# Performance work log

Hardware: AMD Instinct MI355X
Metric: run time of the kernel (lower is better)

Reference implementation:

```python
import jax, jax.numpy as jnp
import numpy as np

B, M = 32768, 200
NUM_LAYERS, OW, OH = 22, 11, 11
CNN_CH, HIDDEN = 128, 512
ACTION_NVEC = (9, 10)


def setup_inputs() -> dict:
    key = jax.random.key(0)
    ks = jax.random.split(key, 16)
    s = 0.02
    inp = {
        "observations": jax.random.randint(ks[0], (B, M, 3), 0, 256, dtype=jnp.int32),
        "max_vec": jnp.ones((NUM_LAYERS,), dtype=jnp.float32),
        "w_conv1": jax.random.normal(ks[1], (CNN_CH, NUM_LAYERS, 5, 5), jnp.float32) * s,
        "b_conv1": jnp.zeros((CNN_CH,), jnp.float32),
        "w_conv2": jax.random.normal(ks[2], (CNN_CH, CNN_CH, 3, 3), jnp.float32) * s,
        "b_conv2": jnp.zeros((CNN_CH,), jnp.float32),
        "w_fc": jax.random.normal(ks[3], (CNN_CH, HIDDEN // 2), jnp.float32) * s,
        "b_fc": jnp.zeros((HIDDEN // 2,), jnp.float32),
        "w_self": jax.random.normal(ks[4], (NUM_LAYERS, HIDDEN // 2), jnp.float32) * s,
        "b_self": jnp.zeros((HIDDEN // 2,), jnp.float32),
        "w_actor0": jax.random.normal(ks[5], (HIDDEN, ACTION_NVEC[0]), jnp.float32) * 0.01,
        "b_actor0": jnp.zeros((ACTION_NVEC[0],), jnp.float32),
        "w_actor1": jax.random.normal(ks[6], (HIDDEN, ACTION_NVEC[1]), jnp.float32) * 0.01,
        "b_actor1": jnp.zeros((ACTION_NVEC[1],), jnp.float32),
        "w_value": jax.random.normal(ks[7], (HIDDEN, 1), jnp.float32) * s,
        "b_value": jnp.zeros((1,), jnp.float32),
    }
    return inp


def _conv(x, w, b, stride):
    y = jax.lax.conv_general_dilated(
        x, w, window_strides=(stride, stride), padding="VALID",
        dimension_numbers=("NCHW", "OIHW", "NCHW"))
    return y + b[None, :, None, None]


def _encode(observations, max_vec, w_conv1, b_conv1, w_conv2, b_conv2,
            w_fc, b_fc, w_self, b_self):
    # torch: token_observations[token_observations == 255] = 0
    obs = jnp.where(observations == 255, 0, observations)
    coords = obs[..., 0]                       # [B, M]
    x_idx = (coords >> 4) & 15
    y_idx = coords & 15
    atr_idx = obs[..., 1]
    atr_val = obs[..., 2].astype(jnp.float32)
    # coords_byte != 255 is always True after the 255->0 rewrite above
    valid = (x_idx < OW) & (y_idx < OH) & (atr_idx < NUM_LAYERS)
    b_idx = jnp.broadcast_to(jnp.arange(obs.shape[0])[:, None], coords.shape)
    # route invalid tokens to a dummy batch slot B, then drop it
    b_idx = jnp.where(valid, b_idx, obs.shape[0])
    a_idx = jnp.where(valid, atr_idx, 0)
    xs = jnp.where(valid, x_idx, 0)
    ys = jnp.where(valid, y_idx, 0)
    box = jnp.zeros((obs.shape[0] + 1, NUM_LAYERS, OW, OH), jnp.float32)
    box = box.at[b_idx, a_idx, xs, ys].set(atr_val)[: obs.shape[0]]
    features = box / max_vec[None, :, None, None]
    self_feat = jax.nn.relu(features[:, :, 5, 5] @ w_self + b_self)   # [B, 256]
    h = jax.nn.relu(_conv(features, w_conv1, b_conv1, 3))             # [B,128,3,3]
    h = jax.nn.relu(_conv(h, w_conv2, b_conv2, 1))                    # [B,128,1,1]
    h = h.reshape(h.shape[0], -1)                                     # [B,128]
    cnn_feat = jax.nn.relu(h @ w_fc + b_fc)                           # [B,256]
    return jnp.concatenate([self_feat, cnn_feat], axis=1)             # [B,512]


def reference(observations, max_vec, w_conv1, b_conv1, w_conv2, b_conv2,
              w_fc, b_fc, w_self, b_self, w_actor0, b_actor0,
              w_actor1, b_actor1, w_value, b_value):
    hidden = _encode(observations, max_vec, w_conv1, b_conv1, w_conv2, b_conv2,
                     w_fc, b_fc, w_self, b_self)
    logits0 = hidden @ w_actor0 + b_actor0
    logits1 = hidden @ w_actor1 + b_actor1
    value = hidden @ w_value + b_value
    return (logits0, logits1, value, hidden)
```

## Files before the change

kernel.cpp:

```cpp
#include <hip/hip_runtime.h>
#include <hip/hip_bf16.h>

typedef unsigned int uint;
typedef unsigned short ushort;
typedef unsigned long long ull;
typedef __attribute__((ext_vector_type(8))) short short8;
typedef __attribute__((ext_vector_type(4))) float float4_;

#define B_TOT 32768
#define NL    22
#define HID0  ((long)B_TOT * 20)

#define W2F_OFF  0
#define WFCF_OFF 294912
#define WHF_OFF  360448
#define W1P_OFF  393216
#define H1_OFF   534016

__device__ __forceinline__ ushort f2bf(float v) {
  uint x = __float_as_uint(v);
  x += 0x7fffu + ((x >> 16) & 1u);
  return (ushort)(x >> 16);
}
__device__ __forceinline__ uint cvtpk(float lo, float hi) {
  uint r;
  asm volatile("v_cvt_pk_bf16_f32 %0, %1, %2" : "=v"(r) : "v"(lo), "v"(hi));
  return r;
}
struct u3 { uint x, y, z; };

extern "C" __global__ __launch_bounds__(256)
void k_prep(const float* __restrict__ wc1, const float* __restrict__ wc2,
            const float* __restrict__ wfc,
            const float* __restrict__ wa0, const float* __restrict__ wa1,
            const float* __restrict__ wv,
            ushort* __restrict__ w2f, ushort* __restrict__ wfcf,
            ushort* __restrict__ whf, uint* __restrict__ w1p)
{
  int i = blockIdx.x * 256 + threadIdx.x;
  if (i < 18432) {
    int l = i & 63, cg = (i >> 6) & 7, ks = i >> 9;
    int col = cg * 16 + (l & 15), kb = ks * 32 + (l >> 4) * 8;
    ushort t[8];
    #pragma unroll
    for (int j = 0; j < 8; ++j) t[j] = f2bf(wc2[col * 1152 + kb + j]);
    uint4 o = { (uint)t[0]|((uint)t[1]<<16), (uint)t[2]|((uint)t[3]<<16),
                (uint)t[4]|((uint)t[5]<<16), (uint)t[6]|((uint)t[7]<<16) };
    ((uint4*)w2f)[i] = o;
  } else if (i < 22528) {
    int i2 = i - 18432;
    int l = i2 & 63, cg = (i2 >> 6) & 15, ks = i2 >> 10;
    int col = cg * 16 + (l & 15), kb = ks * 32 + (l >> 4) * 8;
    ushort t[8];
    #pragma unroll
    for (int j = 0; j < 8; ++j) t[j] = f2bf(wfc[(kb + j) * 256 + col]);
    uint4 o = { (uint)t[0]|((uint)t[1]<<16), (uint)t[2]|((uint)t[3]<<16),
                (uint)t[4]|((uint)t[5]<<16), (uint)t[6]|((uint)t[7]<<16) };
    ((uint4*)wfcf)[i2] = o;
  } else if (i < 24576) {
    int i2 = i - 22528;
    int l = i2 & 63, cg = (i2 >> 6) & 1, ks = i2 >> 7;
    int col = cg * 16 + (l & 15), kb = ks * 32 + (l >> 4) * 8;
    ushort t[8];
    #pragma unroll
    for (int j = 0; j < 8; ++j) {
      int k = kb + j;
      float v = (col < 9)  ? wa0[k*9 + col]
              : (col < 19) ? wa1[k*10 + (col - 9)]
              : (col == 19) ? wv[k] : 0.f;
      t[j] = f2bf(v);
    }
    uint4 o = { (uint)t[0]|((uint)t[1]<<16), (uint)t[2]|((uint)t[3]<<16),
                (uint)t[4]|((uint)t[5]<<16), (uint)t[6]|((uint)t[7]<<16) };
    ((uint4*)whf)[i2] = o;
  } else if (i < 24576 + 35200) {
    int j = i - 24576;
    int l = j & 63, r = j >> 6;
    ushort lo_ = f2bf(wc1[(2*l)     * 550 + r]);
    ushort hi_ = f2bf(wc1[(2*l + 1) * 550 + r]);
    w1p[j] = (uint)lo_ | ((uint)hi_ << 16);
  }
}

#define PROC(cur, acc0, acc1, sav, sbv)                                    \
  {                                                                        \
    int a = (int)((cur) >> 16), x = (int)(((cur) >> 12) & 15u),            \
        y = (int)(((cur) >> 8) & 15u);                                     \
    float rmv = __int_as_float(                                            \
        __builtin_amdgcn_readlane(__float_as_int(rm_own), a));             \
    float fv = (float)((cur) & 255u) * rmv;                                \
    if (x == 5 && y == 5) {                                                \
      const float2* ws2 = (const float2*)(wself + a * 256);                \
      float2 w0 = ws2[lane], w1 = ws2[64 + lane];                          \
      sav.x = fmaf(fv, w0.x, sav.x);  sav.y = fmaf(fv, w0.y, sav.y);       \
      sbv.x = fmaf(fv, w1.x, sbv.x);  sbv.y = fmaf(fv, w1.y, sbv.y);       \
    }                                                                      \
    const int wbase = a * 25;                                              \
    _Pragma("unroll")                                                      \
    for (int ox = 0; ox < 3; ++ox) {                                       \
      int kx = x - 3 * ox;                                                 \
      if ((unsigned)kx > 4u) continue;                                     \
      _Pragma("unroll")                                                    \
      for (int oy = 0; oy < 3; ++oy) {                                     \
        int ky = y - 3 * oy;                                               \
        if ((unsigned)ky > 4u) continue;                                   \
        uint wu = w1p[(wbase + kx * 5 + ky) * 64 + lane];                  \
        float wx = __uint_as_float(wu << 16);                              \
        float wy = __uint_as_float(wu & 0xffff0000u);                      \
        acc0[ox*3+oy] = fmaf(fv, wx, acc0[ox*3+oy]);                       \
        acc1[ox*3+oy] = fmaf(fv, wy, acc1[ox*3+oy]);                       \
      }                                                                    \
    }                                                                      \
  }

#define EPILOG(bS, acc0, acc1, sav, sbv)                                   \
  {                                                                        \
    const float2* bs2 = (const float2*)bself;                              \
    float2 b0_ = bs2[lane], b1_ = bs2[64 + lane];                          \
    float2 o0 = { fmaxf(sav.x + b0_.x, 0.f), fmaxf(sav.y + b0_.y, 0.f) };  \
    float2 o1 = { fmaxf(sbv.x + b1_.x, 0.f), fmaxf(sbv.y + b1_.y, 0.f) };  \
    float2* out2 = (float2*)(out + HID0 + (bS) * 512);                     \
    out2[lane] = o0;                                                       \
    out2[64 + lane] = o1;                                                  \
    const float2 bc = ((const float2*)bc1)[lane];                          \
    float v0[9], v1[9];                                                    \
    _Pragma("unroll")                                                      \
    for (int p = 0; p < 9; ++p) {                                          \
      v0[p] = fmaxf(acc0[p] + bc.x, 0.f);                                  \
      v1[p] = fmaxf(acc1[p] + bc.y, 0.f);                                  \
    }                                                                      \
    uint wds[9];                                                           \
    wds[0] = cvtpk(v0[0], v0[1]);                                          \
    wds[1] = cvtpk(v0[2], v0[3]);                                          \
    wds[2] = cvtpk(v0[4], v0[5]);                                          \
    wds[3] = cvtpk(v0[6], v0[7]);                                          \
    wds[4] = cvtpk(v0[8], v1[0]);                                          \
    wds[5] = cvtpk(v1[1], v1[2]);                                          \
    wds[6] = cvtpk(v1[3], v1[4]);                                          \
    wds[7] = cvtpk(v1[5], v1[6]);                                          \
    wds[8] = cvtpk(v1[7], v1[8]);                                          \
    uint* dst = (uint*)h1g + (bS) * 576 + 9 * lane;                        \
    _Pragma("unroll")                                                      \
    for (int j = 0; j < 9; ++j) dst[j] = wds[j];                           \
  }

extern "C" __global__ __launch_bounds__(256)
void k_encode(const int* __restrict__ obs, const float* __restrict__ maxvec,
              const uint* __restrict__ w1p, const float* __restrict__ bc1,
              const float* __restrict__ wself, const float* __restrict__ bself,
              float* __restrict__ out, ushort* __restrict__ h1g)
{
  __shared__ uint klist[8][64];

  const int tid = threadIdx.x, lane = tid & 63, w = tid >> 6;
  const long bA = (long)blockIdx.x * 8 + w * 2;
  const long bB = bA + 1;

  float rm_own = (lane < NL) ? (1.0f / maxvec[lane]) : 0.f;

  const uint* obA = (const uint*)obs + bA * 600;
  const uint* obB = (const uint*)obs + bB * 600;
  uint* klA = klist[w * 2 + 0];
  uint* klB = klist[w * 2 + 1];

  int cntA = 0, cntB = 0;
  #pragma unroll
  for (int r = 0; r < 4; ++r) {
    int m = r * 64 + lane;
    bool vA = false, vB = false; uint pkA = 0, pkB = 0;
    if (m < 200) {
      u3 tA = *(const u3*)(obA + m * 3);
      u3 tB = *(const u3*)(obB + m * 3);
      uint cA = tA.x, aA = tA.y, vvA = tA.z;
      uint cB = tB.x, aB = tB.y, vvB = tB.z;
      cA = (cA == 255u) ? 0u : cA;  aA = (aA == 255u) ? 0u : aA;  vvA = (vvA == 255u) ? 0u : vvA;
      cB = (cB == 255u) ? 0u : cB;  aB = (aB == 255u) ? 0u : aB;  vvB = (vvB == 255u) ? 0u : vvB;
      uint xA = (cA >> 4) & 15u, yA = cA & 15u;
      uint xB = (cB >> 4) & 15u, yB = cB & 15u;
      vA = (xA < 11u) && (yA < 11u) && (aA < NL);
      vB = (xB < 11u) && (yB < 11u) && (aB < NL);
      pkA = (aA << 16) | (xA << 12) | (yA << 8) | vvA;
      pkB = (aB << 16) | (xB << 12) | (yB << 8) | vvB;
    }
    ull balA = __ballot(vA);
    if (vA) {
      int pos = cntA + __popcll(balA & ((1ull << lane) - 1ull));
      if (pos < 64) klA[pos] = pkA;
    }
    cntA += __popcll(balA);
    ull balB = __ballot(vB);
    if (vB) {
      int pos = cntB + __popcll(balB & ((1ull << lane) - 1ull));
      if (pos < 64) klB[pos] = pkB;
    }
    cntB += __popcll(balB);
  }
  if (cntA > 64) cntA = 64;
  if (cntB > 64) cntB = 64;

  uint uA = (lane < cntA) ? klA[lane] : 0xffffffffu;
  uint uB = (lane < cntB) ? klB[lane] : 0xffffffffu;
  uint cellA = uA >> 8, cellB = uB >> 8;
  bool aliveA = (lane < cntA), aliveB = (lane < cntB);
  const int dmax = (cntA > cntB) ? cntA : cntB;
  for (int d = 1; d < dmax; ++d) {
    uint oA = __shfl_down(cellA, d);
    uint oB = __shfl_down(cellB, d);
    aliveA = aliveA && !((lane + d < cntA) && (oA == cellA));
    aliveB = aliveB && !((lane + d < cntB) && (oB == cellB));
  }
  ull balA2 = __ballot(aliveA);
  const int n2A = __popcll(balA2);
  if (aliveA) klA[__popcll(balA2 & ((1ull << lane) - 1ull))] = uA;
  ull balB2 = __ballot(aliveB);
  const int n2B = __popcll(balB2);
  if (aliveB) klB[__popcll(balB2 & ((1ull << lane) - 1ull))] = uB;

  float aA0[9] = {0,0,0,0,0,0,0,0,0}, aA1[9] = {0,0,0,0,0,0,0,0,0};
  float aB0[9] = {0,0,0,0,0,0,0,0,0}, aB1[9] = {0,0,0,0,0,0,0,0,0};
  float2 saA = {0.f,0.f}, sbA = {0.f,0.f}, saB = {0.f,0.f}, sbB = {0.f,0.f};
  const int tmax = (n2A > n2B) ? n2A : n2B;
  uint nxtA = klA[0], nxtB = klB[0];
  for (int t = 0; t < tmax; ++t) {
    uint curvA = nxtA, curvB = nxtB;
    nxtA = klA[(t + 1) & 63];
    nxtB = klB[(t + 1) & 63];
    uint curA = (uint)__builtin_amdgcn_readfirstlane((int)curvA);
    uint curB = (uint)__builtin_amdgcn_readfirstlane((int)curvB);
    if (t < n2A) PROC(curA, aA0, aA1, saA, sbA);
    if (t < n2B) PROC(curB, aB0, aB1, saB, sbB);
  }

  EPILOG(bA, aA0, aA1, saA, sbA);
  EPILOG(bB, aB0, aB1, saB, sbB);
}

extern "C" __global__ __launch_bounds__(256)
void k_mlp(const ushort* __restrict__ h1g, const ushort* __restrict__ w2f,
           const float* __restrict__ bc2, const ushort* __restrict__ wfcf,
           const float* __restrict__ bfc, const ushort* __restrict__ whf,
           const float* __restrict__ ba0, const float* __restrict__ ba1,
           const float* __restrict__ bv, float* __restrict__ out)
{
  __shared__ short  Abuf[2][4][64][8];
  __shared__ ushort h2A[16][64][8];

  const int tid = threadIdx.x, lane = tid & 63, w = tid >> 6;
  const int lo = lane & 15, hi = lane >> 4;
  const int bb = blockIdx.x, b0 = bb * 64;

  const short8* w2fv  = (const short8*)w2f;
  const short8* wfcfv = (const short8*)wfcf;
  const uint4*  A4    = (const uint4*)h1g;
  const long    arow  = (long)(b0 + (tid >> 2)) * 144 + (tid & 3);

  float4_ acc[4][2];
  #pragma unroll
  for (int cgi = 0; cgi < 2; ++cgi) {
    float bv_ = bc2[(2*w + cgi)*16 + lo];
    float4_ t = {bv_, bv_, bv_, bv_};
    #pragma unroll
    for (int m = 0; m < 4; ++m) acc[m][cgi] = t;
  }

  uint4 rA = A4[arow];
  for (int t = 0; t < 36; ++t) {
    const int cur = t & 1;
    *(uint4*)&Abuf[cur][tid & 3][tid >> 2][0] = rA;
    if (t + 1 < 36) rA = A4[arow + (t + 1) * 4];
    __syncthreads();
    short8 af[4];
    #pragma unroll
    for (int m = 0; m < 4; ++m)
      af[m] = *(const short8*)&Abuf[cur][hi][m*16 + lo][0];
    #pragma unroll
    for (int cgi = 0; cgi < 2; ++cgi) {
      short8 bf = w2fv[(t*8 + 2*w + cgi)*64 + lane];
      #pragma unroll
      for (int m = 0; m < 4; ++m)
        acc[m][cgi] = __builtin_amdgcn_mfma_f32_16x16x32_bf16(af[m], bf, acc[m][cgi], 0, 0, 0);
    }
  }
  __syncthreads();

  #pragma unroll
  for (int cgi = 0; cgi < 2; ++cgi) {
    int col = (2*w + cgi)*16 + lo;
    #pragma unroll
    for (int m = 0; m < 4; ++m)
      #pragma unroll
      for (int q = 0; q < 4; ++q) {
        int R = m*16 + hi*4 + q;
        h2A[col >> 3][R][col & 7] = f2bf(fmaxf(acc[m][cgi][q], 0.f));
      }
  }
  __syncthreads();

  float4_ acc2[4][4];
  #pragma unroll
  for (int cgi = 0; cgi < 4; ++cgi) {
    float bv_ = bfc[(4*w + cgi)*16 + lo];
    float4_ t = {bv_, bv_, bv_, bv_};
    #pragma unroll
    for (int m = 0; m < 4; ++m) acc2[m][cgi] = t;
  }
  #pragma unroll
  for (int ks = 0; ks < 4; ++ks) {
    short8 af[4];
    #pragma unroll
    for (int m = 0; m < 4; ++m)
      af[m] = *(const short8*)&h2A[ks*4 + hi][m*16 + lo][0];
    #pragma unroll
    for (int cgi = 0; cgi < 4; ++cgi) {
      short8 bf = wfcfv[(ks*16 + 4*w + cgi)*64 + lane];
      #pragma unroll
      for (int m = 0; m < 4; ++m)
        acc2[m][cgi] = __builtin_amdgcn_mfma_f32_16x16x32_bf16(af[m], bf, acc2[m][cgi], 0, 0, 0);
    }
  }

  #pragma unroll
  for (int cgi = 0; cgi < 4; ++cgi) {
    int col = (4*w + cgi)*16 + lo;
    #pragma unroll
    for (int m = 0; m < 4; ++m)
      #pragma unroll
      for (int q = 0; q < 4; ++q) {
        int R = m*16 + hi*4 + q;
        out[HID0 + (long)(b0 + R)*512 + 256 + col] = fmaxf(acc2[m][cgi][q], 0.f);
      }
  }
  __syncthreads();

  const short8* whfv = (const short8*)whf;
  float4_ acc3[2];
  #pragma unroll
  for (int cg = 0; cg < 2; ++cg) {
    int col = cg*16 + lo;
    float bias = (col < 9) ? ba0[col] : (col < 19) ? ba1[col - 9]
               : (col == 19) ? bv[0] : 0.f;
    float4_ t = {bias, bias, bias, bias};
    acc3[cg] = t;
  }

  const float* hrow = out + HID0 + (long)(b0 + w*16 + lo) * 512;
  #pragma unroll
  for (int ks = 0; ks < 16; ++ks) {
    float4_ f0 = *(const float4_*)(hrow + ks*32 + hi*8);
    float4_ f1 = *(const float4_*)(hrow + ks*32 + hi*8 + 4);
    union { short8 s; ushort u[8]; } afu;
    afu.u[0] = f2bf(f0[0]); afu.u[1] = f2bf(f0[1]);
    afu.u[2] = f2bf(f0[2]); afu.u[3] = f2bf(f0[3]);
    afu.u[4] = f2bf(f1[0]); afu.u[5] = f2bf(f1[1]);
    afu.u[6] = f2bf(f1[2]); afu.u[7] = f2bf(f1[3]);
    #pragma unroll
    for (int cg = 0; cg < 2; ++cg) {
      short8 bf = whfv[(ks*2 + cg)*64 + lane];
      acc3[cg] = __builtin_amdgcn_mfma_f32_16x16x32_bf16(afu.s, bf, acc3[cg], 0, 0, 0);
    }
  }

  #pragma unroll
  for (int cg = 0; cg < 2; ++cg) {
    int col = cg*16 + lo;
    #pragma unroll
    for (int q = 0; q < 4; ++q) {
      long R = b0 + w*16 + hi*4 + q;
      float v = acc3[cg][q];
      if (col < 9)        out[R*9 + col] = v;
      else if (col < 19)  out[(long)B_TOT*9 + R*10 + (col - 9)] = v;
      else if (col == 19) out[(long)B_TOT*19 + R] = v;
    }
  }
}

extern "C" void kernel_launch(void* const* d_in, const int* in_sizes, int n_in,
                              void* d_out, int out_size, void* d_ws, size_t ws_size,
                              hipStream_t stream) {
  const int* obs      = (const int*)d_in[0];
  const float* maxvec = (const float*)d_in[1];
  const float* wc1    = (const float*)d_in[2];
  const float* bc1    = (const float*)d_in[3];
  const float* wc2    = (const float*)d_in[4];
  const float* bc2    = (const float*)d_in[5];
  const float* wfc    = (const float*)d_in[6];
  const float* bfc    = (const float*)d_in[7];
  const float* wself  = (const float*)d_in[8];
  const float* bself  = (const float*)d_in[9];
  const float* wa0    = (const float*)d_in[10];
  const float* ba0    = (const float*)d_in[11];
  const float* wa1    = (const float*)d_in[12];
  const float* ba1    = (const float*)d_in[13];
  const float* wv     = (const float*)d_in[14];
  const float* bv     = (const float*)d_in[15];
  float* out          = (float*)d_out;

  char* ws = (char*)d_ws;
  ushort* w2f  = (ushort*)(ws + W2F_OFF);
  ushort* wfcf = (ushort*)(ws + WFCF_OFF);
  ushort* whf  = (ushort*)(ws + WHF_OFF);
  uint*   w1p  = (uint*)(ws + W1P_OFF);
  ushort* h1g  = (ushort*)(ws + H1_OFF);

  k_prep  <<<dim3(234),      dim3(256), 0, stream>>>(wc1, wc2, wfc, wa0, wa1, wv,
                                                     w2f, wfcf, whf, w1p);
  k_encode<<<dim3(B_TOT/8),  dim3(256), 0, stream>>>(obs, maxvec, w1p, bc1,
                                                     wself, bself, out, h1g);
  k_mlp   <<<dim3(B_TOT/64), dim3(256), 0, stream>>>(h1g, w2f, bc2, wfcf, bfc,
                                                     whf, ba0, ba1, bv, out);
}
```

Before: 107.0 us.

## Make conv1 scatter loop branch-free using a zero weight row and hoisted self-feature pass

The per-token loop in the encode kernel now always issues all 9 output-position loads and FMAs. Positions outside the kernel window and finished tokens read an appended all-zero weight row (index 550), so the scalar branches on kx/ky and t<n disappear and loads for both samples can be batched. The self-feature accumulation at cell (5,5) moves out of the main loop into a separate ballot-driven pass. This adds redundant FMAs and loads, since only about 1–4 of the 9 positions are valid per token, in exchange for removing divergent control flow and improving load-level parallelism. The weight buffer grows by one row and the H1 offset shifts to match.

Result: slower. 130.6 us (+22.0%).

```diff
diff --git a/kernel.cpp b/kernel.cpp
--- a/kernel.cpp
+++ b/kernel.cpp
@@ -15,7 +15,7 @@
 #define WFCF_OFF 294912
 #define WHF_OFF  360448
 #define W1P_OFF  393216
-#define H1_OFF   534016
+#define H1_OFF   534272
 
 __device__ __forceinline__ ushort f2bf(float v) {
   uint x = __float_as_uint(v);
@@ -73,76 +73,18 @@
     uint4 o = { (uint)t[0]|((uint)t[1]<<16), (uint)t[2]|((uint)t[3]<<16),
                 (uint)t[4]|((uint)t[5]<<16), (uint)t[6]|((uint)t[7]<<16) };
     ((uint4*)whf)[i2] = o;
-  } else if (i < 24576 + 35200) {
+  } else if (i < 24576 + 35264) {
     int j = i - 24576;
     int l = j & 63, r = j >> 6;
-    ushort lo_ = f2bf(wc1[(2*l)     * 550 + r]);
-    ushort hi_ = f2bf(wc1[(2*l + 1) * 550 + r]);
-    w1p[j] = (uint)lo_ | ((uint)hi_ << 16);
-  }
-}
-
-#define PROC(cur, acc0, acc1, sav, sbv)                                    \
-  {                                                                        \
-    int a = (int)((cur) >> 16), x = (int)(((cur) >> 12) & 15u),            \
-        y = (int)(((cur) >> 8) & 15u);                                     \
-    float rmv = __int_as_float(                                            \
-        __builtin_amdgcn_readlane(__float_as_int(rm_own), a));             \
-    float fv = (float)((cur) & 255u) * rmv;                                \
-    if (x == 5 && y == 5) {                                                \
-      const float2* ws2 = (const float2*)(wself + a * 256);                \
-      float2 w0 = ws2[lane], w1 = ws2[64 + lane];                          \
-      sav.x = fmaf(fv, w0.x, sav.x);  sav.y = fmaf(fv, w0.y, sav.y);       \
-      sbv.x = fmaf(fv, w1.x, sbv.x);  sbv.y = fmaf(fv, w1.y, sbv.y);       \
-    }                                                                      \
-    const int wbase = a * 25;                                              \
-    _Pragma("unroll")                                                      \
-    for (int ox = 0; ox < 3; ++ox) {                                       \
-      int kx = x - 3 * ox;                                                 \
-      if ((unsigned)kx > 4u) continue;                                     \
-      _Pragma("unroll")                                                    \
-      for (int oy = 0; oy < 3; ++oy) {                                     \
-        int ky = y - 3 * oy;                                               \
-        if ((unsigned)ky > 4u) continue;                                   \
-        uint wu = w1p[(wbase + kx * 5 + ky) * 64 + lane];                  \
-        float wx = __uint_as_float(wu << 16);                              \
-        float wy = __uint_as_float(wu & 0xffff0000u);                      \
-        acc0[ox*3+oy] = fmaf(fv, wx, acc0[ox*3+oy]);                       \
-        acc1[ox*3+oy] = fmaf(fv, wy, acc1[ox*3+oy]);                       \
-      }                                                                    \
-    }                                                                      \
-  }
-
-#define EPILOG(bS, acc0, acc1, sav, sbv)                                   \
-  {                                                                        \
-    const float2* bs2 = (const float2*)bself;                              \
-    float2 b0_ = bs2[lane], b1_ = bs2[64 + lane];                          \
-    float2 o0 = { fmaxf(sav.x + b0_.x, 0.f), fmaxf(sav.y + b0_.y, 0.f) };  \
-    float2 o1 = { fmaxf(sbv.x + b1_.x, 0.f), fmaxf(sbv.y + b1_.y, 0.f) };  \
-    float2* out2 = (float2*)(out + HID0 + (bS) * 512);                     \
-    out2[lane] = o0;                                                       \
-    out2[64 + lane] = o1;                                                  \
-    const float2 bc = ((const float2*)bc1)[lane];                          \
-    float v0[9], v1[9];                                                    \
-    _Pragma("unroll")                                                      \
-    for (int p = 0; p < 9; ++p) {                                          \
-      v0[p] = fmaxf(acc0[p] + bc.x, 0.f);                                  \
-      v1[p] = fmaxf(acc1[p] + bc.y, 0.f);                                  \
-    }                                                                      \
-    uint wds[9];                                                           \
-    wds[0] = cvtpk(v0[0], v0[1]);                                          \
-    wds[1] = cvtpk(v0[2], v0[3]);                                          \
-    wds[2] = cvtpk(v0[4], v0[5]);                                          \
-    wds[3] = cvtpk(v0[6], v0[7]);                                          \
-    wds[4] = cvtpk(v0[8], v1[0]);                                          \
-    wds[5] = cvtpk(v1[1], v1[2]);                                          \
-    wds[6] = cvtpk(v1[3], v1[4]);                                          \
-    wds[7] = cvtpk(v1[5], v1[6]);                                          \
-    wds[8] = cvtpk(v1[7], v1[8]);                                          \
-    uint* dst = (uint*)h1g + (bS) * 576 + 9 * lane;                        \
-    _Pragma("unroll")                                                      \
-    for (int j = 0; j < 9; ++j) dst[j] = wds[j];                           \
-  }
+    uint val = 0u;
+    if (r < 550) {
+      ushort lo_ = f2bf(wc1[(2*l)     * 550 + r]);
+      ushort hi_ = f2bf(wc1[(2*l + 1) * 550 + r]);
+      val = (uint)lo_ | ((uint)hi_ << 16);
+    }
+    w1p[j] = val;
+  }
+}
 
 extern "C" __global__ __launch_bounds__(256)
 void k_encode(const int* __restrict__ obs, const float* __restrict__ maxvec,
@@ -216,23 +158,114 @@
   const int n2B = __popcll(balB2);
   if (aliveB) klB[__popcll(balB2 & ((1ull << lane) - 1ull))] = uB;
 
+  float2 saA = {0.f,0.f}, sbA = {0.f,0.f}, saB = {0.f,0.f}, sbB = {0.f,0.f};
+  {
+    ull b55A = __ballot(aliveA && (((uA >> 12) & 15u) == 5u) && (((uA >> 8) & 15u) == 5u));
+    while (b55A) {
+      int idx = __builtin_ctzll(b55A); b55A &= b55A - 1ull;
+      uint tk = (uint)__builtin_amdgcn_readlane((int)uA, idx);
+      int a = tk >> 16;
+      float rmv = __int_as_float(__builtin_amdgcn_readlane(__float_as_int(rm_own), a));
+      float fv = (float)(tk & 255u) * rmv;
+      const float2* ws2 = (const float2*)(wself + a * 256);
+      float2 w0 = ws2[lane], w1 = ws2[64 + lane];
+      saA.x = fmaf(fv, w0.x, saA.x);  saA.y = fmaf(fv, w0.y, saA.y);
+      sbA.x = fmaf(fv, w1.x, sbA.x);  sbA.y = fmaf(fv, w1.y, sbA.y);
+    }
+    ull b55B = __ballot(aliveB && (((uB >> 12) & 15u) == 5u) && (((uB >> 8) & 15u) == 5u));
+    while (b55B) {
+      int idx = __builtin_ctzll(b55B); b55B &= b55B - 1ull;
+      uint tk = (uint)__builtin_amdgcn_readlane((int)uB, idx);
+      int a = tk >> 16;
+      float rmv = __int_as_float(__builtin_amdgcn_readlane(__float_as_int(rm_own), a));
+      float fv = (float)(tk & 255u) * rmv;
+      const float2* ws2 = (const float2*)(wself + a * 256);
+      float2 w0 = ws2[lane], w1 = ws2[64 + lane];
+      saB.x = fmaf(fv, w0.x, saB.x);  saB.y = fmaf(fv, w0.y, saB.y);
+      sbB.x = fmaf(fv, w1.x, sbB.x);  sbB.y = fmaf(fv, w1.y, sbB.y);
+    }
+  }
+
   float aA0[9] = {0,0,0,0,0,0,0,0,0}, aA1[9] = {0,0,0,0,0,0,0,0,0};
   float aB0[9] = {0,0,0,0,0,0,0,0,0}, aB1[9] = {0,0,0,0,0,0,0,0,0};
-  float2 saA = {0.f,0.f}, sbA = {0.f,0.f}, saB = {0.f,0.f}, sbB = {0.f,0.f};
   const int tmax = (n2A > n2B) ? n2A : n2B;
   uint nxtA = klA[0], nxtB = klB[0];
   for (int t = 0; t < tmax; ++t) {
     uint curvA = nxtA, curvB = nxtB;
     nxtA = klA[(t + 1) & 63];
     nxtB = klB[(t + 1) & 63];
-    uint curA = (uint)__builtin_amdgcn_readfirstlane((int)curvA);
-    uint curB = (uint)__builtin_amdgcn_readfirstlane((int)curvB);
-    if (t < n2A) PROC(curA, aA0, aA1, saA, sbA);
-    if (t < n2B) PROC(curB, aB0, aB1, saB, sbB);
-  }
-
-  EPILOG(bA, aA0, aA1, saA, sbA);
-  EPILOG(bB, aB0, aB1, saB, sbB);
+    const uint curA = (uint)__builtin_amdgcn_readfirstlane((int)curvA);
+    const uint curB = (uint)__builtin_amdgcn_readfirstlane((int)curvB);
+    const int aAi = curA >> 16, xA = (curA >> 12) & 15, yA = (curA >> 8) & 15;
+    const int aBi = curB >> 16, xB = (curB >> 12) & 15, yB = (curB >> 8) & 15;
+    const bool tvA = (t < n2A), tvB = (t < n2B);
+    float rmvA = __int_as_float(__builtin_amdgcn_readlane(__float_as_int(rm_own), aAi & 63));
+    float rmvB = __int_as_float(__builtin_amdgcn_readlane(__float_as_int(rm_own), aBi & 63));
+    const float fvA = (float)(curA & 255u) * rmvA;
+    const float fvB = (float)(curB & 255u) * rmvB;
+    const int wbaseA = aAi * 25, wbaseB = aBi * 25;
+    #pragma unroll
+    for (int ox = 0; ox < 3; ++ox) {
+      #pragma unroll
+      for (int oy = 0; oy < 3; ++oy) {
+        const int kxA = xA - 3*ox, kyA = yA - 3*oy;
+        const int kxB = xB - 3*ox, kyB = yB - 3*oy;
+        const bool okA = ((unsigned)kxA <= 4u) & ((unsigned)kyA <= 4u) & tvA;
+        const bool okB = ((unsigned)kxB <= 4u) & ((unsigned)kyB <= 4u) & tvB;
+        const int wiA = okA ? (wbaseA + kxA*5 + kyA) : 550;
+        const int wiB = okB ? (wbaseB + kxB*5 + kyB) : 550;
+        const uint wuA = w1p[wiA * 64 + lane];
+        const uint wuB = w1p[wiB * 64 + lane];
+        aA0[ox*3+oy] = fmaf(fvA, __uint_as_float(wuA << 16),         aA0[ox*3+oy]);
+        aA1[ox*3+oy] = fmaf(fvA, __uint_as_float(wuA & 0xffff0000u), aA1[ox*3+oy]);
+        aB0[ox*3+oy] = fmaf(fvB, __uint_as_float(wuB << 16),         aB0[ox*3+oy]);
+        aB1[ox*3+oy] = fmaf(fvB, __uint_as_float(wuB & 0xffff0000u), aB1[ox*3+oy]);
+      }
+    }
+  }
+
+  const float2* bs2 = (const float2*)bself;
+  const float2 bsp0 = bs2[lane], bsp1 = bs2[64 + lane];
+  const float2 bc = ((const float2*)bc1)[lane];
+
+  {
+    float2 o0 = { fmaxf(saA.x + bsp0.x, 0.f), fmaxf(saA.y + bsp0.y, 0.f) };
+    float2 o1 = { fmaxf(sbA.x + bsp1.x, 0.f), fmaxf(sbA.y + bsp1.y, 0.f) };
+    float2* out2 = (float2*)(out + HID0 + bA * 512);
+    out2[lane] = o0;  out2[64 + lane] = o1;
+    uint wds[9];
+    wds[0] = cvtpk(fmaxf(aA0[0]+bc.x,0.f), fmaxf(aA0[1]+bc.x,0.f));
+    wds[1] = cvtpk(fmaxf(aA0[2]+bc.x,0.f), fmaxf(aA0[3]+bc.x,0.f));
+    wds[2] = cvtpk(fmaxf(aA0[4]+bc.x,0.f), fmaxf(aA0[5]+bc.x,0.f));
+    wds[3] = cvtpk(fmaxf(aA0[6]+bc.x,0.f), fmaxf(aA0[7]+bc.x,0.f));
+    wds[4] = cvtpk(fmaxf(aA0[8]+bc.x,0.f), fmaxf(aA1[0]+bc.y,0.f));
+    wds[5] = cvtpk(fmaxf(aA1[1]+bc.y,0.f), fmaxf(aA1[2]+bc.y,0.f));
+    wds[6] = cvtpk(fmaxf(aA1[3]+bc.y,0.f), fmaxf(aA1[4]+bc.y,0.f));
+    wds[7] = cvtpk(fmaxf(aA1[5]+bc.y,0.f), fmaxf(aA1[6]+bc.y,0.f));
+    wds[8] = cvtpk(fmaxf(aA1[7]+bc.y,0.f), fmaxf(aA1[8]+bc.y,0.f));
+    uint* dst = (uint*)h1g + bA * 576 + 9 * lane;
+    #pragma unroll
+    for (int j = 0; j < 9; ++j) dst[j] = wds[j];
+  }
+  {
+    float2 o0 = { fmaxf(saB.x + bsp0.x, 0.f), fmaxf(saB.y + bsp0.y, 0.f) };
+    float2 o1 = { fmaxf(sbB.x + bsp1.x, 0.f), fmaxf(sbB.y + bsp1.y, 0.f) };
+    float2* out2 = (float2*)(out + HID0 + bB * 512);
+    out2[lane] = o0;  out2[64 + lane] = o1;
+    uint wds[9];
+    wds[0] = cvtpk(fmaxf(aB0[0]+bc.x,0.f), fmaxf(aB0[1]+bc.x,0.f));
+    wds[1] = cvtpk(fmaxf(aB0[2]+bc.x,0.f), fmaxf(aB0[3]+bc.x,0.f));
+    wds[2] = cvtpk(fmaxf(aB0[4]+bc.x,0.f), fmaxf(aB0[5]+bc.x,0.f));
+    wds[3] = cvtpk(fmaxf(aB0[6]+bc.x,0.f), fmaxf(aB0[7]+bc.x,0.f));
+    wds[4] = cvtpk(fmaxf(aB0[8]+bc.x,0.f), fmaxf(aB1[0]+bc.y,0.f));
+    wds[5] = cvtpk(fmaxf(aB1[1]+bc.y,0.f), fmaxf(aB1[2]+bc.y,0.f));
+    wds[6] = cvtpk(fmaxf(aB1[3]+bc.y,0.f), fmaxf(aB1[4]+bc.y,0.f));
+    wds[7] = cvtpk(fmaxf(aB1[5]+bc.y,0.f), fmaxf(aB1[6]+bc.y,0.f));
+    wds[8] = cvtpk(fmaxf(aB1[7]+bc.y,0.f), fmaxf(aB1[8]+bc.y,0.f));
+    uint* dst = (uint*)h1g + bB * 576 + 9 * lane;
+    #pragma unroll
+    for (int j = 0; j < 9; ++j) dst[j] = wds[j];
+  }
 }
 
 extern "C" __global__ __launch_bounds__(256)
```
